# Optimization experiments

Hardware: AMD Instinct MI355X
Metric: run time of the kernel (lower is better)

## Reference

```python
import jax, jax.numpy as jnp
import numpy as np

N_NODES = 10000
N_EDGES = 25000
D_FEAT = 128

def setup_inputs() -> dict:
    key = jax.random.key(0)
    k1, k2, k3 = jax.random.split(key, 3)
    x = jax.random.normal(k1, (N_NODES, D_FEAT), dtype=jnp.float32)
    edge_attr = jax.random.normal(k2, (N_EDGES, D_FEAT), dtype=jnp.float32)
    edge_index = jax.random.randint(k3, (2, N_EDGES), 0, N_NODES, dtype=jnp.int64)
    return {"x": x, "edge_attr": edge_attr, "edge_index": edge_index}

def reference(x, edge_attr, edge_index):
    # lg_node_idx: [E, 2] (src, dst) pairs; each original edge becomes a line-graph node
    lg_node_idx = edge_index.T
    # gather endpoint features and average -> [E, d]
    new_x = x[lg_node_idx].mean(axis=1)
    # stack([x, edge_attr], dim=2).mean(dim=2) == elementwise average
    new_x = (new_x + edge_attr) * 0.5
    col0 = lg_node_idx[:, 0]  # src of each edge
    col1 = lg_node_idx[:, 1]  # dst of each edge
    # edge i -> edge j connected iff dst(i) == src(j) and src(i) != dst(j)
    mask = (col1[:, None] == col0[None, :]) & (col0[:, None] != col1[None, :])  # [E, E]
    rows, cols = jnp.nonzero(mask)  # data-dependent size; eager (non-jit) reference
    lg_edge_index = jnp.stack([rows, cols], axis=0)  # [2, E_lg]
    # attr of line-graph edge = feature of shared node's incoming edge's dst entry
    lg_edge_attr_idx = lg_node_idx[rows][:, 1]
    lg_edge_attr = new_x[lg_edge_attr_idx]
    return new_x, lg_edge_index, lg_edge_attr
```

## Files before the change

### kernel.cpp

```cpp
#include <hip/hip_runtime.h>

#define NN 10000
#define NE 25000
#define DF 128
#define SB 256
#define CHUNK 64
#define NCH ((NE + CHUNK - 1) / CHUNK)

typedef float f4 __attribute__((ext_vector_type(4)));

__global__ void k_newx_init(const float* __restrict__ x, const float* __restrict__ ea,
                            const int* __restrict__ c0, const int* __restrict__ c1,
                            float* __restrict__ out, int* __restrict__ head,
                            int* __restrict__ gFlag) {
    int tid = blockIdx.x * blockDim.x + threadIdx.x;
    if (tid < NN) head[tid] = -1;
    if (tid < NCH) gFlag[tid] = 0;
    if (tid >= NE * 32) return;
    int e = tid >> 5, q = tid & 31;
    int u = c0[e], v = c1[e];
    float4 a  = ((const float4*)(x + (size_t)u * DF))[q];
    float4 bb = ((const float4*)(x + (size_t)v * DF))[q];
    float4 c  = ((const float4*)(ea + (size_t)e * DF))[q];
    float4 r;
    r.x = ((a.x + bb.x) * 0.5f + c.x) * 0.5f;
    r.y = ((a.y + bb.y) * 0.5f + c.y) * 0.5f;
    r.z = ((a.z + bb.z) * 0.5f + c.z) * 0.5f;
    r.w = ((a.w + bb.w) * 0.5f + c.w) * 0.5f;
    ((float4*)(out + (size_t)e * DF))[q] = r;
}

__global__ void k_link(const int* __restrict__ c0,
                       int* __restrict__ head, int* __restrict__ nxt) {
    int j = blockIdx.x * blockDim.x + threadIdx.x;
    if (j >= NE) return;
    nxt[j] = atomicExch(&head[c0[j]], j);
}

__global__ __launch_bounds__(1024) void k_scan_emit(
        const float* __restrict__ newx,
        const int* __restrict__ c0, const int* __restrict__ c1,
        const int* __restrict__ head, const int* __restrict__ nxt,
        int* __restrict__ gFlag,
        float* __restrict__ outRows, float* __restrict__ outCols,
        float* __restrict__ outAttr) {
    __shared__ int sCnt[CHUNK];
    __shared__ int sExc[CHUNK];
    __shared__ int sBase;
    int b = blockIdx.x, t = threadIdx.x;
    int wave = t >> 6, lane = t & 63;
    int e0 = b * CHUNK;

    if (wave == 0) {
        int e = e0 + lane;
        int cnt = 0;
        if (e < NE) {
            int u = c0[e], v = c1[e];
            for (int j = head[v]; j != -1; j = nxt[j])
                if (c1[j] != u) ++cnt;
        }
        int incl = cnt;
        for (int off = 1; off < 64; off <<= 1) {
            int vv = __shfl_up(incl, off, 64);
            if (lane >= off) incl += vv;
        }
        int agg = __shfl(incl, 63);
        sCnt[lane] = cnt;
        sExc[lane] = incl - cnt;
        int base = 0;
        if (b == 0) {
            if (lane == 0) atomicExch(&gFlag[0], (2 << 30) | agg);
        } else {
            if (lane == 0) atomicExch(&gFlag[b], (1 << 30) | agg);
            int p = b - 1;
            while (true) {
                int idx = p - lane;
                int st, sm;
                if (idx < 0) { st = 2; sm = 0; }
                else {
                    int f;
                    do {
                        f = __hip_atomic_load(&gFlag[idx], __ATOMIC_ACQUIRE,
                                              __HIP_MEMORY_SCOPE_AGENT);
                        st = (unsigned)f >> 30;
                    } while (st == 0);
                    sm = f & 0x3FFFFFFF;
                }
                unsigned long long inclMask = __ballot(st == 2);
                int contrib;
                if (inclMask) {
                    int l0 = __ffsll(inclMask) - 1;
                    contrib = (lane <= l0) ? sm : 0;
                } else {
                    contrib = sm;
                }
                for (int off = 32; off; off >>= 1)
                    contrib += __shfl_down(contrib, off, 64);
                contrib = __shfl(contrib, 0);
                base += contrib;
                if (inclMask) break;
                p -= 64;
            }
            if (lane == 0) atomicExch(&gFlag[b], (2 << 30) | (base + agg));
        }
        if (lane == 0) sBase = base;
    }
    __syncthreads();

    int gBase = sBase;
    for (int k = 0; k < 4; ++k) {
        int el = wave * 4 + k;
        int i = e0 + el;
        if (i >= NE) break;
        int cnt = sCnt[el];
        if (cnt == 0) continue;
        int base = gBase + sExc[el];
        int u = c0[i], v = c1[i];

        int myj = -1, B = 0;
        for (int j = head[v]; j != -1; j = nxt[j], ++B)
            if (B == lane) myj = j;

        if (B <= 64) {
            int myc1 = (myj >= 0) ? c1[myj] : -1;
            bool keep = (myj >= 0) && (myc1 != u);
            int rank = 0;
            for (int q = 0; q < B; ++q) {
                int jq = __shfl(myj, q);
                int cq = __shfl(myc1, q);
                if (cq != u && jq < myj) ++rank;
            }
            if (keep) {
                __builtin_nontemporal_store((float)i, &outRows[base + rank]);
                __builtin_nontemporal_store((float)myj, &outCols[base + rank]);
            }
        } else {
            int pos = 0;
            for (int j = head[v]; j != -1; j = nxt[j], ++pos) {
                if ((pos & 63) != lane) continue;
                if (c1[j] == u) continue;
                int rank = 0;
                for (int j2 = head[v]; j2 != -1; j2 = nxt[j2])
                    rank += (c1[j2] != u && j2 < j) ? 1 : 0;
                __builtin_nontemporal_store((float)i, &outRows[base + rank]);
                __builtin_nontemporal_store((float)j, &outCols[base + rank]);
            }
        }

        f4 val = ((const f4*)(newx + (size_t)v * DF))[lane & 31];
        for (int tt = (lane >> 5); tt < cnt; tt += 2)
            __builtin_nontemporal_store(val,
                &((f4*)(outAttr + (size_t)(base + tt) * DF))[lane & 31]);
    }
}


extern "C" void kernel_launch(void* const* d_in, const int* in_sizes, int n_in,
                              void* d_out, int out_size, void* d_ws, size_t ws_size,
                              hipStream_t stream) {
    const float* x  = (const float*)d_in[0];
    const float* ea = (const float*)d_in[1];
    const int*   ei = (const int*)d_in[2];
    const int* c0 = ei;
    const int* c1 = ei + NE;

    float* out = (float*)d_out;
    int E_lg = (out_size - NE * DF) / (DF + 2);
    if (E_lg < 0) E_lg = 0;

    float* out_newx = out;
    float* out_rows = out + (size_t)NE * DF;
    float* out_cols = out_rows + E_lg;
    float* out_attr = out_cols + E_lg;

    int* ws    = (int*)d_ws;
    int* head  = ws;
    int* nxt   = head + NN;
    int* gFlag = nxt + NE;

    k_newx_init<<<(NE * 32 + SB - 1) / SB, SB, 0, stream>>>(x, ea, c0, c1, out_newx,
                                                            head, gFlag);
    k_link<<<(NE + SB - 1) / SB, SB, 0, stream>>>(c0, head, nxt);
    k_scan_emit<<<NCH, 1024, 0, stream>>>(out_newx, c0, c1, head, nxt, gFlag,
                                          out_rows, out_cols, out_attr);
}
```

Measured before the change: 44.51 us.

## Restructure scan-emit into persistent blocks with per-wave edge counting and smaller chunks

```diff
diff --git a/kernel.cpp b/kernel.cpp
--- a/kernel.cpp
+++ b/kernel.cpp
@@ -4,8 +4,10 @@
 #define NE 25000
 #define DF 128
 #define SB 256
-#define CHUNK 64
-#define NCH ((NE + CHUNK - 1) / CHUNK)
+#define EPB 8
+#define TPB 512
+#define NCHUNK ((NE + EPB - 1) / EPB)
+#define NPBLK 768
 
 typedef float f4 __attribute__((ext_vector_type(4)));
 
@@ -15,7 +17,7 @@
                             int* __restrict__ gFlag) {
     int tid = blockIdx.x * blockDim.x + threadIdx.x;
     if (tid < NN) head[tid] = -1;
-    if (tid < NCH) gFlag[tid] = 0;
+    if (tid < NCHUNK) gFlag[tid] = 0;
     if (tid >= NE * 32) return;
     int e = tid >> 5, q = tid & 31;
     int u = c0[e], v = c1[e];
@@ -37,120 +39,120 @@
     nxt[j] = atomicExch(&head[c0[j]], j);
 }
 
-__global__ __launch_bounds__(1024) void k_scan_emit(
+__global__ __launch_bounds__(TPB) void k_emit_scan(
         const float* __restrict__ newx,
         const int* __restrict__ c0, const int* __restrict__ c1,
         const int* __restrict__ head, const int* __restrict__ nxt,
         int* __restrict__ gFlag,
         float* __restrict__ outRows, float* __restrict__ outCols,
         float* __restrict__ outAttr) {
-    __shared__ int sCnt[CHUNK];
-    __shared__ int sExc[CHUNK];
+    __shared__ int sCnt[EPB];
+    __shared__ int sExc[EPB];
     __shared__ int sBase;
-    int b = blockIdx.x, t = threadIdx.x;
-    int wave = t >> 6, lane = t & 63;
-    int e0 = b * CHUNK;
+    int wave = threadIdx.x >> 6, lane = threadIdx.x & 63;
 
-    if (wave == 0) {
-        int e = e0 + lane;
-        int cnt = 0;
-        if (e < NE) {
-            int u = c0[e], v = c1[e];
-            for (int j = head[v]; j != -1; j = nxt[j])
-                if (c1[j] != u) ++cnt;
-        }
-        int incl = cnt;
-        for (int off = 1; off < 64; off <<= 1) {
-            int vv = __shfl_up(incl, off, 64);
-            if (lane >= off) incl += vv;
-        }
-        int agg = __shfl(incl, 63);
-        sCnt[lane] = cnt;
-        sExc[lane] = incl - cnt;
-        int base = 0;
-        if (b == 0) {
-            if (lane == 0) atomicExch(&gFlag[0], (2 << 30) | agg);
-        } else {
-            if (lane == 0) atomicExch(&gFlag[b], (1 << 30) | agg);
-            int p = b - 1;
-            while (true) {
-                int idx = p - lane;
-                int st, sm;
-                if (idx < 0) { st = 2; sm = 0; }
-                else {
-                    int f;
-                    do {
-                        f = __hip_atomic_load(&gFlag[idx], __ATOMIC_ACQUIRE,
-                                              __HIP_MEMORY_SCOPE_AGENT);
-                        st = (unsigned)f >> 30;
-                    } while (st == 0);
-                    sm = f & 0x3FFFFFFF;
+    for (int ch = blockIdx.x; ch < NCHUNK; ch += NPBLK) {
+        int i = ch * EPB + wave;
+        int u = 0, v = 0, myj = -1, B = 0, rank = 0, cnt = 0;
+        bool keep = false;
+
+        if (i < NE) {
+            u = c0[i]; v = c1[i];
+            for (int j = head[v]; j != -1; j = nxt[j], ++B)
+                if (B == lane) myj = j;
+            if (B <= 64) {
+                int myc1 = (myj >= 0) ? c1[myj] : -1;
+                keep = (myj >= 0) && (myc1 != u);
+                for (int q = 0; q < B; ++q) {
+                    int jq = __shfl(myj, q);
+                    int cq = __shfl(myc1, q);
+                    if (cq != u && jq < myj) ++rank;
                 }
-                unsigned long long inclMask = __ballot(st == 2);
-                int contrib;
-                if (inclMask) {
-                    int l0 = __ffsll(inclMask) - 1;
-                    contrib = (lane <= l0) ? sm : 0;
-                } else {
-                    contrib = sm;
-                }
-                for (int off = 32; off; off >>= 1)
-                    contrib += __shfl_down(contrib, off, 64);
-                contrib = __shfl(contrib, 0);
-                base += contrib;
-                if (inclMask) break;
-                p -= 64;
-            }
-            if (lane == 0) atomicExch(&gFlag[b], (2 << 30) | (base + agg));
-        }
-        if (lane == 0) sBase = base;
-    }
-    __syncthreads();
-
-    int gBase = sBase;
-    for (int k = 0; k < 4; ++k) {
-        int el = wave * 4 + k;
-        int i = e0 + el;
-        if (i >= NE) break;
-        int cnt = sCnt[el];
-        if (cnt == 0) continue;
-        int base = gBase + sExc[el];
-        int u = c0[i], v = c1[i];
-
-        int myj = -1, B = 0;
-        for (int j = head[v]; j != -1; j = nxt[j], ++B)
-            if (B == lane) myj = j;
-
-        if (B <= 64) {
-            int myc1 = (myj >= 0) ? c1[myj] : -1;
-            bool keep = (myj >= 0) && (myc1 != u);
-            int rank = 0;
-            for (int q = 0; q < B; ++q) {
-                int jq = __shfl(myj, q);
-                int cq = __shfl(myc1, q);
-                if (cq != u && jq < myj) ++rank;
-            }
-            if (keep) {
-                __builtin_nontemporal_store((float)i, &outRows[base + rank]);
-                __builtin_nontemporal_store((float)myj, &outCols[base + rank]);
-            }
-        } else {
-            int pos = 0;
-            for (int j = head[v]; j != -1; j = nxt[j], ++pos) {
-                if ((pos & 63) != lane) continue;
-                if (c1[j] == u) continue;
-                int rank = 0;
-                for (int j2 = head[v]; j2 != -1; j2 = nxt[j2])
-                    rank += (c1[j2] != u && j2 < j) ? 1 : 0;
-                __builtin_nontemporal_store((float)i, &outRows[base + rank]);
-                __builtin_nontemporal_store((float)j, &outCols[base + rank]);
+                cnt = __popcll(__ballot(keep));
+            } else {
+                int c = 0, pos = 0;
+                for (int j = head[v]; j != -1; j = nxt[j], ++pos)
+                    if ((pos & 63) == lane && c1[j] != u) ++c;
+                for (int off = 32; off; off >>= 1) c += __shfl_down(c, off, 64);
+                cnt = __shfl(c, 0);
             }
         }
+        if (lane == 0) sCnt[wave] = cnt;
+        __syncthreads();
 
-        f4 val = ((const f4*)(newx + (size_t)v * DF))[lane & 31];
-        for (int tt = (lane >> 5); tt < cnt; tt += 2)
-            __builtin_nontemporal_store(val,
-                &((f4*)(outAttr + (size_t)(base + tt) * DF))[lane & 31]);
+        if (wave == 0) {
+            int c8 = (lane < EPB) ? sCnt[lane] : 0;
+            for (int off = 1; off < EPB; off <<= 1) {
+                int vv = __shfl_up(c8, off, 64);
+                if (lane >= off) c8 += vv;
+            }
+            int agg = __shfl(c8, EPB - 1);
+            if (lane < EPB) sExc[lane] = c8 - sCnt[lane];
+            int base = 0;
+            if (ch == 0) {
+                if (lane == 0) atomicExch(&gFlag[0], (2 << 30) | agg);
+            } else {
+                if (lane == 0) atomicExch(&gFlag[ch], (1 << 30) | agg);
+                int p = ch - 1;
+                while (true) {
+                    int idx = p - lane;
+                    int st, sm;
+                    if (idx < 0) { st = 2; sm = 0; }
+                    else {
+                        int f;
+                        do {
+                            f = __hip_atomic_load(&gFlag[idx], __ATOMIC_ACQUIRE,
+                                                  __HIP_MEMORY_SCOPE_AGENT);
+                            st = (unsigned)f >> 30;
+                        } while (st == 0);
+                        sm = f & 0x3FFFFFFF;
+                    }
+                    unsigned long long inclMask = __ballot(st == 2);
+                    int contrib;
+                    if (inclMask) {
+                        int l0 = __ffsll(inclMask) - 1;
+                        contrib = (lane <= l0) ? sm : 0;
+                    } else {
+                        contrib = sm;
+                    }
+                    for (int off = 32; off; off >>= 1)
+                        contrib += __shfl_down(contrib, off, 64);
+                    contrib = __shfl(contrib, 0);
+                    base += contrib;
+                    if (inclMask) break;
+                    p -= 64;
+                }
+                if (lane == 0) atomicExch(&gFlag[ch], (2 << 30) | (base + agg));
+            }
+            if (lane == 0) sBase = base;
+        }
+        __syncthreads();
+
+        if (i < NE && cnt > 0) {
+            int base = sBase + sExc[wave];
+            if (B <= 64) {
+                if (keep) {
+                    __builtin_nontemporal_store((float)i, &outRows[base + rank]);
+                    __builtin_nontemporal_store((float)myj, &outCols[base + rank]);
+                }
+            } else {
+                int pos = 0;
+                for (int j = head[v]; j != -1; j = nxt[j], ++pos) {
+                    if ((pos & 63) != lane) continue;
+                    if (c1[j] == u) continue;
+                    int rk = 0;
+                    for (int j2 = head[v]; j2 != -1; j2 = nxt[j2])
+                        rk += (c1[j2] != u && j2 < j) ? 1 : 0;
+                    __builtin_nontemporal_store((float)i, &outRows[base + rk]);
+                    __builtin_nontemporal_store((float)j, &outCols[base + rk]);
+                }
+            }
+            f4 val = ((const f4*)(newx + (size_t)v * DF))[lane & 31];
+            for (int tt = (lane >> 5); tt < cnt; tt += 2)
+                __builtin_nontemporal_store(val,
+                    &((f4*)(outAttr + (size_t)(base + tt) * DF))[lane & 31]);
+        }
+        __syncthreads();
     }
 }
 
@@ -181,6 +183,6 @@
     k_newx_init<<<(NE * 32 + SB - 1) / SB, SB, 0, stream>>>(x, ea, c0, c1, out_newx,
                                                             head, gFlag);
     k_link<<<(NE + SB - 1) / SB, SB, 0, stream>>>(c0, head, nxt);
-    k_scan_emit<<<NCH, 1024, 0, stream>>>(out_newx, c0, c1, head, nxt, gFlag,
-                                          out_rows, out_cols, out_attr);
+    k_emit_scan<<<NPBLK, TPB, 0, stream>>>(out_newx, c0, c1, head, nxt, gFlag,
+                                           out_rows, out_cols, out_attr);
 }
```

Result: slower. 141.9 us (+218.8%).
